# Optimization experiments

Hardware: AMD Instinct MI355X
Metric: run time of the kernel (lower is better)

The kernel has to match this reference:

```python
import jax, jax.numpy as jnp
import numpy as np

V = 20000          # vocab size ('ALL')
E = 512            # embedding_dim
H = 1024           # rnn_hidden_size
LD = 256           # latent_dim
NL = 2             # num_rnn_layers_dec (hidden_factor = 2, unidirectional)
B = 32
S = 256
PAD = 0
CUT0 = 30          # cutoffs = [30, 100, 1000], div_value = 4.0
TAIL_SPECS = [(30, 100, 256), (100, 1000, 64), (1000, V, 16)]  # (low, high, proj_dim)


def setup_inputs() -> dict:
    key = jax.random.key(0)
    ks = jax.random.split(key, 24)
    w = lambda k, shp: (0.02 * jax.random.normal(k, shp)).astype(jnp.float32)

    z = jax.random.normal(ks[0], (B, LD), dtype=jnp.float32)
    emb = w(ks[1], (V, E))
    l2h_w = w(ks[2], (NL * H, LD))
    l2h_b = jnp.zeros((NL * H,), jnp.float32)
    # RNN layer 0 (input E) and layer 1 (input H)
    rnn0_wih = w(ks[3], (H, E)); rnn0_whh = w(ks[4], (H, H))
    rnn0_bih = jnp.zeros((H,), jnp.float32); rnn0_bhh = jnp.zeros((H,), jnp.float32)
    rnn1_wih = w(ks[5], (H, H)); rnn1_whh = w(ks[6], (H, H))
    rnn1_bih = jnp.zeros((H,), jnp.float32); rnn1_bhh = jnp.zeros((H,), jnp.float32)
    # adaptive softmax: head = 30 shortlist + 3 cluster logits
    head_w = w(ks[7], (CUT0 + 3, H))
    tail_p0 = w(ks[8], (256, H));  tail_w0 = w(ks[9], (70, 256))
    tail_p1 = w(ks[10], (64, H));  tail_w1 = w(ks[11], (900, 64))
    tail_p2 = w(ks[12], (16, H));  tail_w2 = w(ks[13], (V - 1000, 16))

    length = jax.random.randint(ks[14], (B,), 32, S + 1)
    pos = jnp.arange(S)[None, :]
    mask = pos < length[:, None]
    inp_seq = jax.random.randint(ks[15], (B, S), 4, V)
    inp_seq = jnp.where(mask, inp_seq, PAD)
    target_seq = jax.random.randint(ks[16], (B, S), 4, V)
    target_seq = jnp.where(mask, target_seq, PAD)

    return dict(z=z, emb=emb, l2h_w=l2h_w, l2h_b=l2h_b,
                rnn0_wih=rnn0_wih, rnn0_whh=rnn0_whh, rnn0_bih=rnn0_bih, rnn0_bhh=rnn0_bhh,
                rnn1_wih=rnn1_wih, rnn1_whh=rnn1_whh, rnn1_bih=rnn1_bih, rnn1_bhh=rnn1_bhh,
                head_w=head_w, tail_p0=tail_p0, tail_w0=tail_w0, tail_p1=tail_p1,
                tail_w1=tail_w1, tail_p2=tail_p2, tail_w2=tail_w2,
                inp_seq=inp_seq, target_seq=target_seq, length=length)


def _rnn_layer(x, h0, wih, whh, bih, bhh):
    # x: [B,S,D], h0: [B,H] -> [B,S,H]  (tanh vanilla RNN)
    def step(h, xt):
        h = jnp.tanh(xt @ wih.T + bih + h @ whh.T + bhh)
        return h, h
    _, ys = jax.lax.scan(step, h0, jnp.swapaxes(x, 0, 1))
    return jnp.swapaxes(ys, 0, 1)


def _adaptive_log_prob(x, head_w, tails):
    # x: [N,H] -> full log-probs [N,V] (AdaptiveLogSoftmaxWithLoss.log_prob)
    head_lp = jax.nn.log_softmax(x @ head_w.T, axis=-1)  # [N, 33]
    parts = [head_lp[:, :CUT0]]
    for i, (p, w) in enumerate(tails):
        clp = jax.nn.log_softmax((x @ p.T) @ w.T, axis=-1)
        parts.append(clp + head_lp[:, CUT0 + i][:, None])
    return jnp.concatenate(parts, axis=1)


def reference(z, emb, l2h_w, l2h_b,
              rnn0_wih, rnn0_whh, rnn0_bih, rnn0_bhh,
              rnn1_wih, rnn1_whh, rnn1_bih, rnn1_bhh,
              head_w, tail_p0, tail_w0, tail_p1, tail_w1, tail_p2, tail_w2,
              inp_seq, target_seq, length):
    # sort inputs by descending length (hidden is NOT sorted, as in the original)
    sorted_idx = jnp.argsort(-length)
    x = emb[inp_seq[sorted_idx]]                         # [B,S,E]
    hid = z @ l2h_w.T + l2h_b                            # [B, 2H]
    hidden = hid.reshape(NL, B, H)                       # torch .view(hidden_factor, B, H)
    h1 = _rnn_layer(x, hidden[0], rnn0_wih, rnn0_whh, rnn0_bih, rnn0_bhh)
    h2 = _rnn_layer(h1, hidden[1], rnn1_wih, rnn1_whh, rnn1_bih, rnn1_bhh)
    rev = jnp.argsort(sorted_idx)
    out = h2[rev].reshape(-1, H)                         # [N,H]
    tgt = target_seq.reshape(-1)                         # [N]
    lp = _adaptive_log_prob(out, head_w,
                            [(tail_p0, tail_w0), (tail_p1, tail_w1), (tail_p2, tail_w2)])
    nll = -jnp.take_along_axis(lp, tgt[:, None], axis=1)[:, 0]
    nll = jnp.where(tgt == PAD, 0.0, nll)
    return jnp.sum(nll)
```

## Files before the change

### kernel.cpp

```cpp
#include <hip/hip_runtime.h>
#include <hip/hip_bf16.h>
#include <math.h>

#define BB 32
#define SS 256
#define EE 512
#define HH 1024
#define LDM 256
#define NROW (BB*SS)
#define NWG 64

typedef __attribute__((ext_vector_type(8))) short bf16x8;
typedef __attribute__((ext_vector_type(4))) float f32x4;
typedef unsigned long long u64;

static __device__ inline unsigned short f2bf(float f){
  unsigned u = __float_as_uint(f);
  unsigned r = (u + 0x7fffu + ((u >> 16) & 1u)) >> 16;
  return (unsigned short)r;
}
static __device__ inline unsigned short f2bf_fast(float f){
  return (unsigned short)((__float_as_uint(f) + 0x8000u) >> 16);
}
static __device__ inline bf16x8 cvt8(float4 x, float4 y){
  union { ushort s[8]; bf16x8 v; } t;
  t.s[0]=f2bf_fast(x.x); t.s[1]=f2bf_fast(x.y); t.s[2]=f2bf_fast(x.z); t.s[3]=f2bf_fast(x.w);
  t.s[4]=f2bf_fast(y.x); t.s[5]=f2bf_fast(y.y); t.s[6]=f2bf_fast(y.z); t.s[7]=f2bf_fast(y.w);
  return t.v;
}
static __device__ inline unsigned packbf(float a, float b){
  return (unsigned)f2bf(a) | ((unsigned)f2bf(b) << 16);
}

static __device__ inline float ftanh(float x){
  float e = __expf(2.f*x);
  return 1.f - 2.f/(e + 1.f);
}

#define GLD(dst, p) asm volatile("global_load_dwordx4 %0, %1, off sc0 sc1" \
                                 : "=v"(dst) : "v"(p) : "memory")

static __device__ inline bf16x8 asbf(f32x4 x){
  union { f32x4 f; bf16x8 b; } u; u.f = x; return u.b;
}

__global__ void k_sort(const int* __restrict__ length, int* __restrict__ sorted_idx){
  int b = threadIdx.x;
  if (b >= BB) return;
  int lb = length[b];
  int r = 0;
  for (int o = 0; o < BB; ++o){
    int lo = length[o];
    if (lo > lb || (lo == lb && o < b)) ++r;
  }
  sorted_idx[r] = b;
}

__global__ void k_maps(const int* __restrict__ sorted_idx,
                       const int* __restrict__ inp_seq, const int* __restrict__ tgt_seq,
                       int* __restrict__ tokmap, int* __restrict__ tgtmap){
  int bs = blockIdx.x; int t = threadIdx.x;
  int b = sorted_idx[bs];
  tokmap[bs*SS + t] = inp_seq[b*SS + t];
  tgtmap[bs*SS + t] = tgt_seq[b*SS + t];
}

__global__ __launch_bounds__(256) void k_hid(const float* __restrict__ z,
        const float* __restrict__ w, const float* __restrict__ bias,
        ushort* __restrict__ hb0){
  int id = blockIdx.x*256 + threadIdx.x;
  int b = id >> 11, c = id & 2047;
  const float4* zr = (const float4*)(z + b*LDM);
  const float4* wr = (const float4*)(w + (size_t)c*LDM);
  float a0=0,a1=0,a2=0,a3=0;
  #pragma unroll 4
  for (int k=0;k<LDM/4;k++){ float4 zz=zr[k], ww=wr[k];
    a0+=zz.x*ww.x; a1+=zz.y*ww.y; a2+=zz.z*ww.z; a3+=zz.w*ww.w; }
  float val = a0+a1+a2+a3 + bias[c];
  int layer = id >> 15, bp = (id >> 10) & 31, j = id & 1023;
  hb0[(layer<<15) + ((j>>3)<<8) + (bp<<3) + (j&7)] = f2bf(val);
}

__global__ __launch_bounds__(256) void k_wcat(
    const float* __restrict__ head_w, const float* __restrict__ p0,
    const float* __restrict__ p1, const float* __restrict__ p2,
    float* __restrict__ wcat){
  int row = blockIdx.x; int t = threadIdx.x;
  float4* dst = (float4*)(wcat + (size_t)row*HH);
  const float* src;
  if      (row < 33)  src = head_w + (size_t)row*HH;
  else if (row < 289) src = p0 + (size_t)(row-33)*HH;
  else if (row < 353) src = p1 + (size_t)(row-289)*HH;
  else if (row < 369) src = p2 + (size_t)(row-353)*HH;
  else { dst[t] = make_float4(0.f,0.f,0.f,0.f); return; }
  dst[t] = ((const float4*)src)[t];
}

__global__ __launch_bounds__(256) void k_bin(
    const int* __restrict__ tgtmap, int* __restrict__ cnt,
    int* __restrict__ l0, int* __restrict__ l1, int* __restrict__ l2)
{
  int row = blockIdx.x*256 + threadIdx.x;
  int tgt = tgtmap[row];
  int ci = (tgt == 0) ? -1 : (tgt >= 1000) ? 2 : (tgt >= 100) ? 1 : (tgt >= 30) ? 0 : -1;
  int lane = threadIdx.x & 63;
  #pragma unroll
  for (int c = 0; c < 3; ++c){
    unsigned long long mask = __ballot(ci == c);
    int nc = __popcll(mask);
    int base = 0;
    if (lane == 0 && nc) base = atomicAdd(&cnt[c], nc);
    base = __shfl(base, 0);
    if (ci == c){
      int pos = __popcll(mask & ((1ull << lane) - 1ull));
      int* lst = (c == 0) ? l0 : (c == 1) ? l1 : l2;
      lst[base + pos] = row;
    }
  }
}

__global__ __launch_bounds__(256) void k_gemm_bf16(
    const float* __restrict__ A, int lda, const int* __restrict__ rowmap,
    const float* __restrict__ Bm,
    const float* __restrict__ bias0, const float* __restrict__ bias1,
    float* __restrict__ C, int M, int N, int K)
{
  __shared__ ushort As[128*72];
  __shared__ ushort Bs[128*72];
  const int nt = blockIdx.x * 128, mt = blockIdx.y * 128;
  const int tid = threadIdx.x;
  const int wv = tid >> 6, ln = tid & 63;
  const int wm = wv & 1, wn = wv >> 1;
  const int lc = ln & 15, quad = ln >> 4;
  f32x4 acc[4][4] = {{{0.f,0.f,0.f,0.f}}};

  for (int s = 0; s < K; s += 64){
    __syncthreads();
    #pragma unroll
    for (int cc = 0; cc < 4; ++cc){
      int ch = tid*4 + cc;
      int r = ch >> 3, c = ch & 7;
      int ar = mt + r;
      const float* ap = A + (size_t)(rowmap ? rowmap[ar] : ar)*lda + s + c*8;
      float4 x = *(const float4*)ap, y = *(const float4*)(ap+4);
      *(bf16x8*)&As[r*72 + c*8] = cvt8(x, y);
      int br = nt + r; if (br >= N) br = N - 1;
      const float* bp = Bm + (size_t)br*K + s + c*8;
      float4 bx = *(const float4*)bp, by = *(const float4*)(bp+4);
      *(bf16x8*)&Bs[r*72 + c*8] = cvt8(bx, by);
    }
    __syncthreads();
    #pragma unroll
    for (int kq = 0; kq < 2; ++kq){
      int cq = kq*4 + quad;
      bf16x8 af[4], bfv[4];
      #pragma unroll
      for (int i=0;i<4;i++) af[i]  = *(const bf16x8*)&As[(wm*64 + i*16 + lc)*72 + cq*8];
      #pragma unroll
      for (int j=0;j<4;j++) bfv[j] = *(const bf16x8*)&Bs[(wn*64 + j*16 + lc)*72 + cq*8];
      #pragma unroll
      for (int i=0;i<4;i++)
        #pragma unroll
        for (int j=0;j<4;j++)
          acc[i][j] = __builtin_amdgcn_mfma_f32_16x16x32_bf16(af[i], bfv[j], acc[i][j], 0, 0, 0);
    }
  }
  #pragma unroll
  for (int j=0;j<4;j++){
    int col = nt + wn*64 + j*16 + lc;
    if (col < N){
      float badd = (bias0 ? bias0[col] : 0.f) + (bias1 ? bias1[col] : 0.f);
      #pragma unroll
      for (int i=0;i<4;i++){
        int row = mt + wm*64 + i*16 + quad*4;
        #pragma unroll
        for (int r=0;r<4;r++)
          C[(size_t)(row+r)*N + col] = acc[i][j][r] + badd;
      }
    }
  }
}

__global__ __launch_bounds__(256, 1) void k_rnn_fused(
    const float* __restrict__ pre0, float* __restrict__ h2out,
    const float* __restrict__ w0hh, const float* __restrict__ w1ih,
    const float* __restrict__ w1hh,
    const float* __restrict__ b1ih, const float* __restrict__ b1hh,
    const ushort* __restrict__ hb0, ushort* __restrict__ hx, int* flags)
{
  __shared__ ushort w0F[16384], wiF[16384], whF[16384];
  __shared__ float red[4352];
  const int wg  = blockIdx.x;
  const int tid = threadIdx.x;
  const int j0  = wg * 16;
  int* ctr = flags + (wg & 7) * 32;

  for (int c = tid; c < 4096; c += 256){
    int rr = c >> 8, cc = (c & 255) * 4;
    int dst = ((cc >> 3)*16 + rr)*8 + (cc & 7);
    size_t srow = (size_t)(j0 + rr)*HH + cc;
    float4 w4; uint2 p;
    w4 = *(const float4*)&w0hh[srow];
    p.x = packbf(w4.x, w4.y); p.y = packbf(w4.z, w4.w);
    *(uint2*)&w0F[dst] = p;
    w4 = *(const float4*)&w1ih[srow];
    p.x = packbf(w4.x, w4.y); p.y = packbf(w4.z, w4.w);
    *(uint2*)&wiF[dst] = p;
    w4 = *(const float4*)&w1hh[srow];
    p.x = packbf(w4.x, w4.y); p.y = packbf(w4.z, w4.w);
    *(uint2*)&whF[dst] = p;
  }
  const int lane = tid & 63, wv = tid >> 6;
  const int col = lane & 15, quad = lane >> 4;
  const int ob = tid >> 3, oj = (tid << 1) & 15;

  float2 pre = *(const float2*)&pre0[((size_t)ob*SS + 0)*HH + j0 + oj];
  float2 pre2;
  pre2.x = b1ih[j0+oj]   + b1hh[j0+oj];
  pre2.y = b1ih[j0+oj+1] + b1hh[j0+oj+1];
  __syncthreads();

  for (int r = 0; r < SS; ++r){
    const u64* s1 = (const u64*)(r == 0 ? hb0 : hx + ((r-1)&1)*32768);
    const u64* s2 = (r == 0) ? (const u64*)hb0
                  : (const u64*)(r == 1 ? hb0 + 32768 : hx + (2 + (r&1))*32768);
    f32x4 a0r[8], a1r[8], c0r[8], c1r[8];
    #pragma unroll
    for (int ks = 0; ks < 8; ++ks){
      int kb = wv*32 + ks*4 + quad;
      const u64* p = s1 + (kb << 6) + (col << 1);
      GLD(a0r[ks], p);
      GLD(a1r[ks], p + 32);
    }
    if (r > 0){
      #pragma unroll
      for (int ks = 0; ks < 8; ++ks){
        int kb = wv*32 + ks*4 + quad;
        const u64* p = s2 + (kb << 6) + (col << 1);
        GLD(c0r[ks], p);
        GLD(c1r[ks], p + 32);
      }
    }
    asm volatile("s_waitcnt vmcnt(0)" ::: "memory");
    __builtin_amdgcn_sched_barrier(0);

    f32x4 accA0 = {0.f,0.f,0.f,0.f}, accA1 = {0.f,0.f,0.f,0.f};
    f32x4 accB0 = {0.f,0.f,0.f,0.f}, accB1 = {0.f,0.f,0.f,0.f};
    #pragma unroll
    for (int ks = 0; ks < 8; ++ks){
      int kb = wv*32 + ks*4 + quad;
      bf16x8 b0 = *(const bf16x8*)&w0F[(kb*16 + col)*8];
      accA0 = __builtin_amdgcn_mfma_f32_16x16x32_bf16(asbf(a0r[ks]), b0, accA0, 0, 0, 0);
      accA1 = __builtin_amdgcn_mfma_f32_16x16x32_bf16(asbf(a1r[ks]), b0, accA1, 0, 0, 0);
      bf16x8 bi = *(const bf16x8*)&wiF[(kb*16 + col)*8];
      accB0 = __builtin_amdgcn_mfma_f32_16x16x32_bf16(asbf(a0r[ks]), bi, accB0, 0, 0, 0);
      accB1 = __builtin_amdgcn_mfma_f32_16x16x32_bf16(asbf(a1r[ks]), bi, accB1, 0, 0, 0);
    }
    if (r > 0){
      #pragma unroll
      for (int ks = 0; ks < 8; ++ks){
        int kb = wv*32 + ks*4 + quad;
        bf16x8 bh = *(const bf16x8*)&whF[(kb*16 + col)*8];
        accB0 = __builtin_amdgcn_mfma_f32_16x16x32_bf16(asbf(c0r[ks]), bh, accB0, 0, 0, 0);
        accB1 = __builtin_amdgcn_mfma_f32_16x16x32_bf16(asbf(c1r[ks]), bh, accB1, 0, 0, 0);
      }
    }
    #pragma unroll
    for (int q = 0; q < 4; ++q){
      red[wv*544 + (quad*4 + q)*17 + col]             = accA0[q];
      red[wv*544 + (16 + quad*4 + q)*17 + col]        = accA1[q];
      red[2176 + wv*544 + (quad*4 + q)*17 + col]      = accB0[q];
      red[2176 + wv*544 + (16 + quad*4 + q)*17 + col] = accB1[q];
    }
    __syncthreads();

    int ro = ob*17 + oj;
    float s0 = red[ro]   + red[544 + ro]   + red[1088 + ro]   + red[1632 + ro];
    float s1v= red[ro+1] + red[544 + ro+1] + red[1088 + ro+1] + red[1632 + ro+1];
    float v0 = ftanh(pre.x + s0);
    float v1 = ftanh(pre.y + s1v);
    int k = j0 + oj;
    unsigned off = ((unsigned)(k >> 3) << 7) + ((unsigned)ob << 2) + ((unsigned)(k & 7) >> 1);
    __hip_atomic_store((unsigned*)(hx + (r&1)*32768) + off, packbf(v0, v1),
                       __ATOMIC_RELAXED, __HIP_MEMORY_SCOPE_AGENT);
    float w0v = 0.f, w1v = 0.f;
    if (r > 0){
      float s2v = red[2176+ro]   + red[2720+ro]   + red[3264+ro]   + red[3808+ro];
      float s3v = red[2176+ro+1] + red[2720+ro+1] + red[3264+ro+1] + red[3808+ro+1];
      w0v = ftanh(pre2.x + s2v);
      w1v = ftanh(pre2.y + s3v);
      __hip_atomic_store((unsigned*)(hx + (2 + ((r-1)&1))*32768) + off, packbf(w0v, w1v),
                         __ATOMIC_RELAXED, __HIP_MEMORY_SCOPE_AGENT);
    }
    asm volatile("s_waitcnt vmcnt(0)" ::: "memory");
    __syncthreads();
    if (tid == 0)
      __hip_atomic_fetch_add(ctr, 1, __ATOMIC_RELAXED, __HIP_MEMORY_SCOPE_AGENT);

    if (r > 0)
      *(float2*)&h2out[((size_t)ob*SS + (r-1))*HH + j0 + oj] = make_float2(w0v, w1v);
    int tn = (r + 1 < SS) ? r + 1 : SS - 1;
    pre = *(const float2*)&pre0[((size_t)ob*SS + tn)*HH + j0 + oj];

    if (tid < 8){
      int tv = 8 * (r + 1);
      while (__hip_atomic_load(flags + tid*32, __ATOMIC_RELAXED,
                               __HIP_MEMORY_SCOPE_AGENT) < tv) {}
    }
    __syncthreads();
  }

  {
    const u64* s1 = (const u64*)(hx + 32768);
    const u64* s2 = (const u64*)(hx + 2*32768);
    f32x4 a0r[8], a1r[8], c0r[8], c1r[8];
    #pragma unroll
    for (int ks = 0; ks < 8; ++ks){
      int kb = wv*32 + ks*4 + quad;
      const u64* p1 = s1 + (kb << 6) + (col << 1);
      GLD(a0r[ks], p1); GLD(a1r[ks], p1 + 32);
      const u64* p2 = s2 + (kb << 6) + (col << 1);
      GLD(c0r[ks], p2); GLD(c1r[ks], p2 + 32);
    }
    asm volatile("s_waitcnt vmcnt(0)" ::: "memory");
    __builtin_amdgcn_sched_barrier(0);
    f32x4 accB0 = {0.f,0.f,0.f,0.f}, accB1 = {0.f,0.f,0.f,0.f};
    #pragma unroll
    for (int ks = 0; ks < 8; ++ks){
      int kb = wv*32 + ks*4 + quad;
      bf16x8 bi = *(const bf16x8*)&wiF[(kb*16 + col)*8];
      accB0 = __builtin_amdgcn_mfma_f32_16x16x32_bf16(asbf(a0r[ks]), bi, accB0, 0, 0, 0);
      accB1 = __builtin_amdgcn_mfma_f32_16x16x32_bf16(asbf(a1r[ks]), bi, accB1, 0, 0, 0);
      bf16x8 bh = *(const bf16x8*)&whF[(kb*16 + col)*8];
      accB0 = __builtin_amdgcn_mfma_f32_16x16x32_bf16(asbf(c0r[ks]), bh, accB0, 0, 0, 0);
      accB1 = __builtin_amdgcn_mfma_f32_16x16x32_bf16(asbf(c1r[ks]), bh, accB1, 0, 0, 0);
    }
    #pragma unroll
    for (int q = 0; q < 4; ++q){
      red[wv*544 + (quad*4 + q)*17 + col]      = accB0[q];
      red[wv*544 + (16 + quad*4 + q)*17 + col] = accB1[q];
    }
    __syncthreads();
    int ro = ob*17 + oj;
    float s2v = red[ro]   + red[544 + ro]   + red[1088 + ro]   + red[1632 + ro];
    float s3v = red[ro+1] + red[544 + ro+1] + red[1088 + ro+1] + red[1632 + ro+1];
    *(float2*)&h2out[((size_t)ob*SS + (SS-1))*HH + j0 + oj] =
        make_float2(ftanh(pre2.x + s2v), ftanh(pre2.y + s3v));
  }
}

__global__ __launch_bounds__(256) void k_cluster(
    const float* __restrict__ combo, int off, int ld, int Kp,
    const float* __restrict__ W, int Nc,
    const int* __restrict__ rowlist, const int* __restrict__ cntp, int ci,
    float* __restrict__ stats)
{
  __shared__ float ps[4][4][256];
  int lane = threadIdx.x & 63;
  int wvl  = threadIdx.x >> 6;
  int n0 = (blockIdx.x*4 + wvl) * 4;
  int count = cntp[ci];
  int rows[4];
  #pragma unroll
  for (int r=0;r<4;r++){
    rows[r] = (n0 + r < count) ? rowlist[n0 + r] : -1;
    if (rows[r] >= 0)
      for (int k=lane;k<Kp;k+=64)
        ps[wvl][r][k] = combo[(size_t)rows[r]*ld + off + k];
  }
  __syncthreads();
  if (rows[0] < 0) return;

  float mx[4], sm[4];
  #pragma unroll
  for (int r=0;r<4;r++){ mx[r]=-1e30f; sm[r]=0.f; }
  for (int n=lane; n<Nc; n+=64){
    const float* wr = W + (size_t)n*Kp;
    float l[4]={0.f,0.f,0.f,0.f};
    for (int k=0;k<Kp;k+=4){
      float4 w4 = *(const float4*)(wr+k);
      #pragma unroll
      for (int r=0;r<4;r++){
        l[r] += w4.x*ps[wvl][r][k] + w4.y*ps[wvl][r][k+1]
              + w4.z*ps[wvl][r][k+2] + w4.w*ps[wvl][r][k+3];
      }
    }
    #pragma unroll
    for (int r=0;r<4;r++){
      float nm = fmaxf(mx[r], l[r]);
      sm[r] = sm[r]*__expf(mx[r]-nm) + __expf(l[r]-nm);
      mx[r] = nm;
    }
  }
  #pragma unroll
  for (int r=0;r<4;r++){
    for (int off2=32; off2; off2>>=1){
      float om = __shfl_down(mx[r], off2);
      float os = __shfl_down(sm[r], off2);
      float nm = fmaxf(mx[r], om);
      sm[r] = sm[r]*__expf(mx[r]-nm) + os*__expf(om-nm);
      mx[r] = nm;
    }
    if (lane==0 && rows[r] >= 0){
      stats[(size_t)rows[r]*6 + ci*2 + 0] = mx[r];
      stats[(size_t)rows[r]*6 + ci*2 + 1] = sm[r];
    }
  }
}

__global__ __launch_bounds__(256) void k_tlogit(
    const int* __restrict__ tgtmap, const float* __restrict__ combo,
    const float* __restrict__ w0, const float* __restrict__ w1, const float* __restrict__ w2,
    float* __restrict__ tlogit)
{
  int lane = threadIdx.x & 63;
  int row = (blockIdx.x * 256 + threadIdx.x) >> 6;
  int tgt = tgtmap[row];
  float acc = 0.f;
  const float* pr = nullptr; const float* wr = nullptr; int Kp = 0;
  const float* crow = combo + (size_t)row*384;
  if      (tgt >= 1000){ pr = crow + 353; wr = w2 + (size_t)(tgt-1000)*16;  Kp=16;  }
  else if (tgt >= 100) { pr = crow + 289; wr = w1 + (size_t)(tgt-100)*64;   Kp=64;  }
  else if (tgt >= 30)  { pr = crow + 33;  wr = w0 + (size_t)(tgt-30)*256;   Kp=256; }
  for (int k=lane; k<Kp; k+=64) acc += pr[k]*wr[k];
  for (int off=32; off; off>>=1) acc += __shfl_down(acc, off);
  if (lane==0) tlogit[row] = acc;
}

__global__ __launch_bounds__(256) void k_final(
    const float* __restrict__ combo, const float* __restrict__ stats,
    const float* __restrict__ tlogit, const int* __restrict__ tgtmap,
    float* __restrict__ out)
{
  int row = blockIdx.x*256 + threadIdx.x;
  int tgt = tgtmap[row];
  float nll = 0.f;
  if (tgt != 0){
    const float* hrow = combo + (size_t)row*384;
    float m = hrow[0];
    #pragma unroll
    for (int i=1;i<33;i++) m = fmaxf(m, hrow[i]);
    float s = 0.f;
    #pragma unroll
    for (int i=0;i<33;i++) s += __expf(hrow[i]-m);
    float lse = __logf(s) + m;
    int ci = (tgt>=1000) ? 2 : (tgt>=100) ? 1 : (tgt>=30) ? 0 : -1;
    if (ci < 0){
      nll = lse - hrow[tgt];
    } else {
      float cm = stats[(size_t)row*6 + ci*2 + 0];
      float cs = stats[(size_t)row*6 + ci*2 + 1];
      nll = lse - hrow[30+ci] + (__logf(cs) + cm - tlogit[row]);
    }
  }
  float v = nll;
  for (int off=32; off; off>>=1) v += __shfl_down(v, off);
  __shared__ float wsum[4];
  int lane = threadIdx.x & 63, wv = threadIdx.x >> 6;
  if (lane==0) wsum[wv] = v;
  __syncthreads();
  if (threadIdx.x==0) atomicAdd(out, wsum[0]+wsum[1]+wsum[2]+wsum[3]);
}

extern "C" void kernel_launch(void* const* d_in, const int* in_sizes, int n_in,
                              void* d_out, int out_size, void* d_ws, size_t ws_size,
                              hipStream_t stream)
{
  const float* z      = (const float*)d_in[0];
  const float* emb    = (const float*)d_in[1];
  const float* l2h_w  = (const float*)d_in[2];
  const float* l2h_b  = (const float*)d_in[3];
  const float* w0ih   = (const float*)d_in[4];
  const float* w0hh   = (const float*)d_in[5];
  const float* b0ih   = (const float*)d_in[6];
  const float* b0hh   = (const float*)d_in[7];
  const float* w1ih   = (const float*)d_in[8];
  const float* w1hh   = (const float*)d_in[9];
  const float* b1ih   = (const float*)d_in[10];
  const float* b1hh   = (const float*)d_in[11];
  const float* head_w = (const float*)d_in[12];
  const float* p0     = (const float*)d_in[13];
  const float* tw0    = (const float*)d_in[14];
  const float* p1     = (const float*)d_in[15];
  const float* tw1    = (const float*)d_in[16];
  const float* p2     = (const float*)d_in[17];
  const float* tw2    = (const float*)d_in[18];
  const int* inp_seq  = (const int*)d_in[19];
  const int* tgt_seq  = (const int*)d_in[20];
  const int* length   = (const int*)d_in[21];

  float* ws   = (float*)d_ws;
  ushort* hb0 = (ushort*)ws;
  ushort* hx  = hb0 + 65536;
  float* bufA = ws + 98304;
  float* bufB = bufA + (size_t)NROW*HH;
  int*   ibuf = (int*)(bufB + (size_t)NROW*HH);
  int* sorted_idx = ibuf;
  int* tokmap = ibuf + 32;
  int* tgtmap = tokmap + NROW;
  int* flags  = tgtmap + NROW;
  int* bincnt = flags + 512;
  int* blist0 = bincnt + 32;
  int* blist1 = blist0 + NROW;
  int* blist2 = blist1 + NROW;
  float* combo = bufA;
  float* stats = bufA + (size_t)NROW*384;
  float* tlog  = stats + (size_t)NROW*6;
  float* wcat  = tlog + NROW;

  float* outF = (float*)d_out;
  hipMemsetAsync(outF, 0, sizeof(float), stream);
  hipMemsetAsync(flags, 0, 544*sizeof(int), stream);

  k_sort<<<1, 32, 0, stream>>>(length, sorted_idx);
  k_maps<<<32, 256, 0, stream>>>(sorted_idx, inp_seq, tgt_seq, tokmap, tgtmap);
  k_hid<<<256, 256, 0, stream>>>(z, l2h_w, l2h_b, hb0);
  k_bin<<<32, 256, 0, stream>>>(tgtmap, bincnt, blist0, blist1, blist2);

  k_gemm_bf16<<<dim3(HH/128, NROW/128), 256, 0, stream>>>(emb, EE, tokmap, w0ih,
                                                          b0ih, b0hh, bufA, NROW, HH, EE);
  k_rnn_fused<<<NWG, 256, 0, stream>>>(bufA, bufB, w0hh, w1ih, w1hh, b1ih, b1hh,
                                       hb0, hx, flags);

  k_wcat<<<384, 256, 0, stream>>>(head_w, p0, p1, p2, wcat);
  k_gemm_bf16<<<dim3(3, NROW/128), 256, 0, stream>>>(bufB, HH, nullptr, wcat,
                                                     nullptr, nullptr, combo, NROW, 384, HH);

  k_cluster<<<NROW/16, 256, 0, stream>>>(combo, 33,  384, 256, tw0, 70,
                                         blist0, bincnt, 0, stats);
  k_cluster<<<NROW/16, 256, 0, stream>>>(combo, 289, 384, 64,  tw1, 900,
                                         blist1, bincnt, 1, stats);
  k_cluster<<<NROW/16, 256, 0, stream>>>(combo, 353, 384, 16,  tw2, 19000,
                                         blist2, bincnt, 2, stats);
  k_tlogit<<<NROW/4, 256, 0, stream>>>(tgtmap, combo, tw0, tw1, tw2, tlog);
  k_final<<<NROW/256, 256, 0, stream>>>(combo, stats, tlog, tgtmap, outF);
}
```

Baseline: 1.564 ms.

## Store RNN output as bf16, widen cluster rows per wave, pipeline flag polling

The fused RNN kernel now writes its layer-2 hidden states as packed bf16 instead of fp32. The follow-on GEMM gains a flag so it reads this bf16 A operand directly, which halves that traffic and drops the conversion step. The cluster log-sum-exp kernel now handles 8 rows per wave instead of 4, so each weight row read is reused across more rows, at the cost of more registers and shared memory. The spin-wait on inter-workgroup flags also keeps two loads in flight to cut polling latency.

```diff
diff --git a/kernel.cpp b/kernel.cpp
--- a/kernel.cpp
+++ b/kernel.cpp
@@ -120,7 +120,7 @@
 }
 
 __global__ __launch_bounds__(256) void k_gemm_bf16(
-    const float* __restrict__ A, int lda, const int* __restrict__ rowmap,
+    const float* __restrict__ A, int lda, const int* __restrict__ rowmap, int abf16,
     const float* __restrict__ Bm,
     const float* __restrict__ bias0, const float* __restrict__ bias1,
     float* __restrict__ C, int M, int N, int K)
@@ -141,9 +141,14 @@
       int ch = tid*4 + cc;
       int r = ch >> 3, c = ch & 7;
       int ar = mt + r;
-      const float* ap = A + (size_t)(rowmap ? rowmap[ar] : ar)*lda + s + c*8;
-      float4 x = *(const float4*)ap, y = *(const float4*)(ap+4);
-      *(bf16x8*)&As[r*72 + c*8] = cvt8(x, y);
+      if (abf16){
+        const ushort* ap = (const ushort*)A + (size_t)ar*lda + s + c*8;
+        *(bf16x8*)&As[r*72 + c*8] = *(const bf16x8*)ap;
+      } else {
+        const float* ap = A + (size_t)(rowmap ? rowmap[ar] : ar)*lda + s + c*8;
+        float4 x = *(const float4*)ap, y = *(const float4*)(ap+4);
+        *(bf16x8*)&As[r*72 + c*8] = cvt8(x, y);
+      }
       int br = nt + r; if (br >= N) br = N - 1;
       const float* bp = Bm + (size_t)br*K + s + c*8;
       float4 bx = *(const float4*)bp, by = *(const float4*)(bp+4);
@@ -182,7 +187,7 @@
 }
 
 __global__ __launch_bounds__(256, 1) void k_rnn_fused(
-    const float* __restrict__ pre0, float* __restrict__ h2out,
+    const float* __restrict__ pre0, ushort* __restrict__ h2out,
     const float* __restrict__ w0hh, const float* __restrict__ w1ih,
     const float* __restrict__ w1hh,
     const float* __restrict__ b1ih, const float* __restrict__ b1hh,
@@ -283,13 +288,12 @@
     unsigned off = ((unsigned)(k >> 3) << 7) + ((unsigned)ob << 2) + ((unsigned)(k & 7) >> 1);
     __hip_atomic_store((unsigned*)(hx + (r&1)*32768) + off, packbf(v0, v1),
                        __ATOMIC_RELAXED, __HIP_MEMORY_SCOPE_AGENT);
-    float w0v = 0.f, w1v = 0.f;
+    unsigned pk2 = 0;
     if (r > 0){
       float s2v = red[2176+ro]   + red[2720+ro]   + red[3264+ro]   + red[3808+ro];
       float s3v = red[2176+ro+1] + red[2720+ro+1] + red[3264+ro+1] + red[3808+ro+1];
-      w0v = ftanh(pre2.x + s2v);
-      w1v = ftanh(pre2.y + s3v);
-      __hip_atomic_store((unsigned*)(hx + (2 + ((r-1)&1))*32768) + off, packbf(w0v, w1v),
+      pk2 = packbf(ftanh(pre2.x + s2v), ftanh(pre2.y + s3v));
+      __hip_atomic_store((unsigned*)(hx + (2 + ((r-1)&1))*32768) + off, pk2,
                          __ATOMIC_RELAXED, __HIP_MEMORY_SCOPE_AGENT);
     }
     asm volatile("s_waitcnt vmcnt(0)" ::: "memory");
@@ -298,14 +302,19 @@
       __hip_atomic_fetch_add(ctr, 1, __ATOMIC_RELAXED, __HIP_MEMORY_SCOPE_AGENT);
 
     if (r > 0)
-      *(float2*)&h2out[((size_t)ob*SS + (r-1))*HH + j0 + oj] = make_float2(w0v, w1v);
+      *((unsigned*)h2out + (((size_t)ob*SS + (r-1))*HH + j0 + oj) / 2) = pk2;
     int tn = (r + 1 < SS) ? r + 1 : SS - 1;
     pre = *(const float2*)&pre0[((size_t)ob*SS + tn)*HH + j0 + oj];
 
     if (tid < 8){
       int tv = 8 * (r + 1);
-      while (__hip_atomic_load(flags + tid*32, __ATOMIC_RELAXED,
-                               __HIP_MEMORY_SCOPE_AGENT) < tv) {}
+      const int* fp = flags + tid*32;
+      int va = __hip_atomic_load(fp, __ATOMIC_RELAXED, __HIP_MEMORY_SCOPE_AGENT);
+      int vb = __hip_atomic_load(fp, __ATOMIC_RELAXED, __HIP_MEMORY_SCOPE_AGENT);
+      while (va < tv){
+        va = vb;
+        vb = __hip_atomic_load(fp, __ATOMIC_RELAXED, __HIP_MEMORY_SCOPE_AGENT);
+      }
     }
     __syncthreads();
   }
@@ -344,8 +353,8 @@
     int ro = ob*17 + oj;
     float s2v = red[ro]   + red[544 + ro]   + red[1088 + ro]   + red[1632 + ro];
     float s3v = red[ro+1] + red[544 + ro+1] + red[1088 + ro+1] + red[1632 + ro+1];
-    *(float2*)&h2out[((size_t)ob*SS + (SS-1))*HH + j0 + oj] =
-        make_float2(ftanh(pre2.x + s2v), ftanh(pre2.y + s3v));
+    *((unsigned*)h2out + (((size_t)ob*SS + (SS-1))*HH + j0 + oj) / 2) =
+        packbf(ftanh(pre2.x + s2v), ftanh(pre2.y + s3v));
   }
 }
 
@@ -355,14 +364,14 @@
     const int* __restrict__ rowlist, const int* __restrict__ cntp, int ci,
     float* __restrict__ stats)
 {
-  __shared__ float ps[4][4][256];
+  __shared__ float ps[4][8][256];
   int lane = threadIdx.x & 63;
   int wvl  = threadIdx.x >> 6;
-  int n0 = (blockIdx.x*4 + wvl) * 4;
+  int n0 = (blockIdx.x*4 + wvl) * 8;
   int count = cntp[ci];
-  int rows[4];
+  int rows[8];
   #pragma unroll
-  for (int r=0;r<4;r++){
+  for (int r=0;r<8;r++){
     rows[r] = (n0 + r < count) ? rowlist[n0 + r] : -1;
     if (rows[r] >= 0)
       for (int k=lane;k<Kp;k+=64)
@@ -371,29 +380,29 @@
   __syncthreads();
   if (rows[0] < 0) return;
 
-  float mx[4], sm[4];
+  float mx[8], sm[8];
   #pragma unroll
-  for (int r=0;r<4;r++){ mx[r]=-1e30f; sm[r]=0.f; }
+  for (int r=0;r<8;r++){ mx[r]=-1e30f; sm[r]=0.f; }
   for (int n=lane; n<Nc; n+=64){
     const float* wr = W + (size_t)n*Kp;
-    float l[4]={0.f,0.f,0.f,0.f};
+    float l[8]={0.f,0.f,0.f,0.f,0.f,0.f,0.f,0.f};
     for (int k=0;k<Kp;k+=4){
       float4 w4 = *(const float4*)(wr+k);
       #pragma unroll
-      for (int r=0;r<4;r++){
+      for (int r=0;r<8;r++){
         l[r] += w4.x*ps[wvl][r][k] + w4.y*ps[wvl][r][k+1]
               + w4.z*ps[wvl][r][k+2] + w4.w*ps[wvl][r][k+3];
       }
     }
     #pragma unroll
-    for (int r=0;r<4;r++){
+    for (int r=0;r<8;r++){
       float nm = fmaxf(mx[r], l[r]);
       sm[r] = sm[r]*__expf(mx[r]-nm) + __expf(l[r]-nm);
       mx[r] = nm;
     }
   }
   #pragma unroll
-  for (int r=0;r<4;r++){
+  for (int r=0;r<8;r++){
     for (int off2=32; off2; off2>>=1){
       float om = __shfl_down(mx[r], off2);
       float os = __shfl_down(sm[r], off2);
@@ -493,8 +502,8 @@
   ushort* hb0 = (ushort*)ws;
   ushort* hx  = hb0 + 65536;
   float* bufA = ws + 98304;
-  float* bufB = bufA + (size_t)NROW*HH;
-  int*   ibuf = (int*)(bufB + (size_t)NROW*HH);
+  ushort* hbB = (ushort*)(bufA + (size_t)NROW*HH);
+  int*   ibuf = (int*)(hbB + (size_t)NROW*HH);
   int* sorted_idx = ibuf;
   int* tokmap = ibuf + 32;
   int* tgtmap = tokmap + NROW;
@@ -517,20 +526,21 @@
   k_hid<<<256, 256, 0, stream>>>(z, l2h_w, l2h_b, hb0);
   k_bin<<<32, 256, 0, stream>>>(tgtmap, bincnt, blist0, blist1, blist2);
 
-  k_gemm_bf16<<<dim3(HH/128, NROW/128), 256, 0, stream>>>(emb, EE, tokmap, w0ih,
+  k_gemm_bf16<<<dim3(HH/128, NROW/128), 256, 0, stream>>>(emb, EE, tokmap, 0, w0ih,
                                                           b0ih, b0hh, bufA, NROW, HH, EE);
-  k_rnn_fused<<<NWG, 256, 0, stream>>>(bufA, bufB, w0hh, w1ih, w1hh, b1ih, b1hh,
+  k_rnn_fused<<<NWG, 256, 0, stream>>>(bufA, hbB, w0hh, w1ih, w1hh, b1ih, b1hh,
                                        hb0, hx, flags);
 
   k_wcat<<<384, 256, 0, stream>>>(head_w, p0, p1, p2, wcat);
-  k_gemm_bf16<<<dim3(3, NROW/128), 256, 0, stream>>>(bufB, HH, nullptr, wcat,
-                                                     nullptr, nullptr, combo, NROW, 384, HH);
-
-  k_cluster<<<NROW/16, 256, 0, stream>>>(combo, 33,  384, 256, tw0, 70,
+  k_gemm_bf16<<<dim3(3, NROW/128), 256, 0, stream>>>((const float*)hbB, HH, nullptr, 1,
+                                                     wcat, nullptr, nullptr,
+                                                     combo, NROW, 384, HH);
+
+  k_cluster<<<NROW/32, 256, 0, stream>>>(combo, 33,  384, 256, tw0, 70,
                                          blist0, bincnt, 0, stats);
-  k_cluster<<<NROW/16, 256, 0, stream>>>(combo, 289, 384, 64,  tw1, 900,
+  k_cluster<<<NROW/32, 256, 0, stream>>>(combo, 289, 384, 64,  tw1, 900,
                                          blist1, bincnt, 1, stats);
-  k_cluster<<<NROW/16, 256, 0, stream>>>(combo, 353, 384, 16,  tw2, 19000,
+  k_cluster<<<NROW/32, 256, 0, stream>>>(combo, 353, 384, 16,  tw2, 19000,
                                          blist2, bincnt, 2, stats);
   k_tlogit<<<NROW/4, 256, 0, stream>>>(tgtmap, combo, tw0, tw1, tw2, tlog);
   k_final<<<NROW/256, 256, 0, stream>>>(combo, stats, tlog, tgtmap, outF);
```

Result: slower. 1.680 ms (+7.4%).
